# Kernel optimization log

Hardware: AMD Instinct MI355X
Metric: run time of the kernel (lower is better)

The kernel has to match this reference:

```python
import jax, jax.numpy as jnp
import numpy as np

TOP_K = 8
N_GROUP = 8
TOPK_GROUP = 4
ROUTED_SCALE = 2.5


def setup_inputs() -> dict:
    key = jax.random.key(0)
    ks = jax.random.split(key, 7)
    T, H, E, I, SI = 4096, 1024, 32, 512, 2048
    W = 0.05  # weight scale to keep relu^2 activations sane
    return {
        "hidden_states": jax.random.normal(ks[0], (T, H), jnp.float32),
        "gate_w": jax.random.normal(ks[1], (E, H), jnp.float32) * W,
        "bias": jax.random.normal(ks[2], (E,), jnp.float32),
        "w_up": jax.random.normal(ks[3], (E, I, H), jnp.float32) * W,
        "w_down": jax.random.normal(ks[4], (E, H, I), jnp.float32) * W,
        "shared_up": jax.random.normal(ks[5], (SI, H), jnp.float32) * W,
        "shared_down": jax.random.normal(ks[6], (H, SI), jnp.float32) * W,
    }


def _grouped_topk_sigmoid(logits, bias):
    # vLLM grouped_topk with scoring_func='sigmoid' + e_score_correction_bias
    T, E = logits.shape
    scores = jax.nn.sigmoid(logits)                       # [T, E]
    sfc = scores + bias[None, :]                          # scores for choice
    g = sfc.reshape(T, N_GROUP, E // N_GROUP)
    group_scores = jnp.sum(jax.lax.top_k(g, 2)[0], -1)    # [T, G] sum of top-2
    grp_idx = jax.lax.top_k(group_scores, TOPK_GROUP)[1]  # [T, topk_group]
    gmask = jnp.zeros((T, N_GROUP), bool).at[jnp.arange(T)[:, None], grp_idx].set(True)
    emask = jnp.repeat(gmask, E // N_GROUP, axis=1)       # [T, E]
    masked = jnp.where(emask, sfc, -jnp.inf)
    topk_ids = jax.lax.top_k(masked, TOP_K)[1]            # [T, K]
    topk_w = jnp.take_along_axis(scores, topk_ids, axis=1)  # weights from raw scores
    topk_w = topk_w / jnp.sum(topk_w, axis=-1, keepdims=True)  # renormalize
    return topk_w, topk_ids


def reference(hidden_states, gate_w, bias, w_up, w_down, shared_up, shared_down):
    x = hidden_states
    T, H = x.shape
    E = gate_w.shape[0]
    # router (fp32 gate)
    logits = x.astype(jnp.float32) @ gate_w.T
    topk_w, topk_ids = _grouped_topk_sigmoid(logits, bias)
    # dense combine weights [T, E] (zero for unselected experts)
    gates = jnp.zeros((T, E), x.dtype).at[jnp.arange(T)[:, None], topk_ids].set(
        topk_w.astype(x.dtype))
    # routed experts: relu^2 MLP (no gating mul), combined with gate weights
    h = jnp.einsum('th,eih->tei', x, w_up)                # [T, E, I]
    h = jnp.square(jax.nn.relu(h))
    routed = jnp.einsum('tei,te,ehi->th', h, gates, w_down)
    # shared expert (same relu^2 MLP)
    s = jnp.square(jax.nn.relu(x @ shared_up.T)) @ shared_down.T
    return routed * ROUTED_SCALE + s
```

## Files before the change

kernel.cpp:

```cpp
#include <hip/hip_runtime.h>
#include <hip/hip_bf16.h>


typedef _Float16 h8 __attribute__((ext_vector_type(8)));
typedef _Float16 h4 __attribute__((ext_vector_type(4)));
typedef float f4 __attribute__((ext_vector_type(4)));

#define T_TOK 4096
#define HDIM  1024
#define NEXP  32
#define IDIM  512
#define SIDIM 2048
#define TOPK  8
#define MAXTU 224
#define MAXTD 160

__device__ __forceinline__ void gload16(const void* g, void* l) {
    __builtin_amdgcn_global_load_lds(
        (const __attribute__((address_space(1))) void*)g,
        (__attribute__((address_space(3))) void*)l, 16, 0, 0);
}

__global__ __launch_bounds__(256) void cvt_all_kernel(
    const float* __restrict__ sA, _Float16* __restrict__ dA, int nA,
    const float* __restrict__ sB, _Float16* __restrict__ dB, int nB,
    const float* __restrict__ sC, _Float16* __restrict__ dC, int nC,
    const float* __restrict__ sD, _Float16* __restrict__ dD, int nD,
    const float* __restrict__ sE, _Float16* __restrict__ dE, int nE) {
    const int total = nA + nB + nC + nD + nE;
    for (int gi = blockIdx.x * 256 + threadIdx.x; gi < total; gi += gridDim.x * 256) {
        const float* s; _Float16* d; int i = gi;
        if (i < nA) { s = sA; d = dA; }
        else { i -= nA;
        if (i < nB) { s = sB; d = dB; }
        else { i -= nB;
        if (i < nC) { s = sC; d = dC; }
        else { i -= nC;
        if (i < nD) { s = sD; d = dD; }
        else { i -= nD; s = sE; d = dE; } } } }
        float4 v = reinterpret_cast<const float4*>(s)[i];
        h4 h; h[0] = (_Float16)v.x; h[1] = (_Float16)v.y; h[2] = (_Float16)v.z; h[3] = (_Float16)v.w;
        reinterpret_cast<h4*>(d)[i] = h;
    }
}

__global__ __launch_bounds__(256) void logits_select_kernel(
    const float* __restrict__ x, const float* __restrict__ gw,
    const float* __restrict__ bias, int* __restrict__ topk_ids,
    float* __restrict__ topk_w) {
    const int t0  = blockIdx.x * 16;
    const int tid = threadIdx.x;
    __shared__ double xS[16][66];
    __shared__ double gS[32][65];
    __shared__ double sS[16][33];
    __shared__ double sfcS[16][33];
    const int e  = tid & 31;
    const int tg = tid >> 5;
    const int tA = tg * 2, tB = tg * 2 + 1;
    double acc0 = 0.0, acc1 = 0.0;

    for (int kc = 0; kc < HDIM; kc += 64) {
        {
            int r = tid >> 4, c0 = (tid & 15) * 4;
            float4 v = *reinterpret_cast<const float4*>(x + (size_t)(t0 + r) * HDIM + kc + c0);
            xS[r][c0]     = (double)v.x;
            xS[r][c0 + 1] = (double)v.y;
            xS[r][c0 + 2] = (double)v.z;
            xS[r][c0 + 3] = (double)v.w;
        }
        {
            int r = tid >> 3, c0 = (tid & 7) * 8;
            const float* gp = gw + (size_t)r * HDIM + kc + c0;
            float4 v0 = *reinterpret_cast<const float4*>(gp);
            float4 v1 = *reinterpret_cast<const float4*>(gp + 4);
            gS[r][c0]     = (double)v0.x;
            gS[r][c0 + 1] = (double)v0.y;
            gS[r][c0 + 2] = (double)v0.z;
            gS[r][c0 + 3] = (double)v0.w;
            gS[r][c0 + 4] = (double)v1.x;
            gS[r][c0 + 5] = (double)v1.y;
            gS[r][c0 + 6] = (double)v1.z;
            gS[r][c0 + 7] = (double)v1.w;
        }
        __syncthreads();
#pragma unroll
        for (int k = 0; k < 64; ++k) {
            double g = gS[e][k];
            acc0 = fma(g, xS[tA][k], acc0);
            acc1 = fma(g, xS[tB][k], acc1);
        }
        __syncthreads();
    }
    {
        double s0 = 1.0 / (1.0 + exp(-acc0));
        double s1 = 1.0 / (1.0 + exp(-acc1));
        double b = (double)bias[e];
        sS[tA][e] = s0;  sfcS[tA][e] = s0 + b;
        sS[tB][e] = s1;  sfcS[tB][e] = s1 + b;
    }
    __syncthreads();

    if (tid < 16) {
        const int t = t0 + tid;
        double gsc[8];
        for (int g = 0; g < 8; ++g) {
            double m1 = -1e300, m2 = -1e300;
            for (int j = 0; j < 4; ++j) {
                double v = sfcS[tid][g * 4 + j];
                if (v > m1) { m2 = m1; m1 = v; } else if (v > m2) { m2 = v; }
            }
            gsc[g] = m1 + m2;
        }
        bool gsel[8] = {};
        for (int r = 0; r < 4; ++r) {
            int best = 0; double bv = -1e300;
            for (int g = 0; g < 8; ++g)
                if (!gsel[g] && gsc[g] > bv) { bv = gsc[g]; best = g; }
            gsel[best] = true;
        }
        bool esel[32];
        for (int i2 = 0; i2 < 32; ++i2) esel[i2] = false;
        int ids[8]; double wsum = 0.0;
        for (int r = 0; r < 8; ++r) {
            int best = 0; double bv = -1e300;
            for (int e2 = 0; e2 < 32; ++e2)
                if (gsel[e2 >> 2] && !esel[e2] && sfcS[tid][e2] > bv) { bv = sfcS[tid][e2]; best = e2; }
            esel[best] = true;
            ids[r] = best;
            wsum += sS[tid][best];
        }
        for (int r = 0; r < 8; ++r) {
            topk_ids[t * TOPK + r] = ids[r];
            topk_w[t * TOPK + r] = (float)(sS[tid][ids[r]] / wsum * 2.5);
        }
    }
}

__global__ void build_lists_kernel(const int* __restrict__ ids, const float* __restrict__ w,
                                   int* __restrict__ tok_list, float* __restrict__ wt_list,
                                   int* __restrict__ dest_list, int* __restrict__ counts) {
    const int e = blockIdx.x;
    const int lane = threadIdx.x;
    int base = 0;
    for (int t0 = 0; t0 < T_TOK; t0 += 64) {
        int t = t0 + lane;
        int found = -1;
#pragma unroll
        for (int k = 0; k < TOPK; ++k)
            if (ids[t * TOPK + k] == e) found = k;
        unsigned long long mask = __ballot(found >= 0);
        if (found >= 0) {
            int pos = base + __popcll(mask & ((1ull << lane) - 1ull));
            tok_list[e * T_TOK + pos]  = t;
            wt_list[e * T_TOK + pos]   = w[t * TOPK + found];
            dest_list[e * T_TOK + pos] = t * TOPK + found;
        }
        base += __popcll(mask);
    }
    if (lane == 0) counts[e] = base;
}

__global__ void scan_offsets_kernel(const int* __restrict__ counts, int* __restrict__ offsets,
                                    int* __restrict__ tmapU, int* __restrict__ tmapD) {
    if (threadIdx.x == 0) {
        int run = 0, ntu = 0, ntd = 0;
        for (int e = 0; e < NEXP; ++e) {
            offsets[e] = run;
            for (int m0 = 0; m0 < counts[e]; m0 += 256) {
                tmapU[1 + 2 * ntu] = e; tmapU[2 + 2 * ntu] = m0; ++ntu;
                tmapD[1 + 2 * ntd] = e; tmapD[2 + 2 * ntd] = m0; ++ntd;
            }
            run += counts[e];
        }
        offsets[NEXP] = run;
        for (int c = 0; c < 4; ++c)
            for (int m0 = 0; m0 < T_TOK; m0 += 256) {
                tmapU[1 + 2 * ntu] = NEXP + c; tmapU[2 + 2 * ntu] = m0; ++ntu;
            }
        tmapU[0] = ntu;
        tmapD[0] = ntd;
    }
}

__device__ __forceinline__ void gemm8p(const _Float16* const (&aP)[4],
                                       const _Float16* const (&bP)[4],
                                       const int nt, f4 (&acc)[8][4]) {
    __shared__ __attribute__((aligned(16))) _Float16 As[2][256 * 64];
    __shared__ __attribute__((aligned(16))) _Float16 Bs[2][256 * 64];
    const int tid = threadIdx.x;
    const int w = tid >> 6, lane = tid & 63;
    const int wr = w >> 2, wc = w & 3;
    const int ra = lane & 15, kq = lane >> 4;
    const int ldsb = w * 512;
    const int arow = wr * 128 + ra;
    const int brow = wc * 64 + ra;
    const int ch0 = (kq ^ (ra & 7)) << 3;
    const int ch1 = ((4 + kq) ^ (ra & 7)) << 3;

#pragma unroll
    for (int j = 0; j < 4; ++j) gload16(aP[j], &As[0][j * 4096 + ldsb]);
#pragma unroll
    for (int j = 0; j < 4; ++j) gload16(bP[j], &Bs[0][j * 4096 + ldsb]);

    for (int t = 0; t < nt; ++t) {
        const int buf = t & 1, nb = buf ^ 1;
        const bool pf = (t + 1 < nt);
        const int ko = (t + 1) * 64;

        asm volatile("s_waitcnt vmcnt(0)" ::: "memory");
        __builtin_amdgcn_s_barrier();
        asm volatile("" ::: "memory");

        h8 bf0[4], af0[4];
#pragma unroll
        for (int n = 0; n < 4; ++n)
            bf0[n] = *reinterpret_cast<const h8*>(&Bs[buf][(brow + n * 16) * 64 + ch0]);
#pragma unroll
        for (int m = 0; m < 4; ++m)
            af0[m] = *reinterpret_cast<const h8*>(&As[buf][(arow + m * 16) * 64 + ch0]);
        if (pf) {
            gload16(aP[0] + ko, &As[nb][0 * 4096 + ldsb]);
            gload16(aP[1] + ko, &As[nb][1 * 4096 + ldsb]);
        }
        h8 af1[4];
#pragma unroll
        for (int m = 0; m < 4; ++m)
            af1[m] = *reinterpret_cast<const h8*>(&As[buf][(arow + (m + 4) * 16) * 64 + ch0]);
        if (pf) {
            gload16(aP[2] + ko, &As[nb][2 * 4096 + ldsb]);
            gload16(aP[3] + ko, &As[nb][3 * 4096 + ldsb]);
        }
        __builtin_amdgcn_s_setprio(1);
#pragma unroll
        for (int m = 0; m < 4; ++m)
#pragma unroll
            for (int n = 0; n < 4; ++n)
                acc[m][n] = __builtin_amdgcn_mfma_f32_16x16x32_f16(af0[m], bf0[n], acc[m][n], 0, 0, 0);
        __builtin_amdgcn_s_setprio(0);
        if (pf) {
            gload16(bP[0] + ko, &Bs[nb][0 * 4096 + ldsb]);
            gload16(bP[1] + ko, &Bs[nb][1 * 4096 + ldsb]);
        }
        h8 bf1[4], af2[4];
#pragma unroll
        for (int n = 0; n < 4; ++n)
            bf1[n] = *reinterpret_cast<const h8*>(&Bs[buf][(brow + n * 16) * 64 + ch1]);
#pragma unroll
        for (int m = 0; m < 4; ++m)
            af2[m] = *reinterpret_cast<const h8*>(&As[buf][(arow + m * 16) * 64 + ch1]);
        __builtin_amdgcn_s_setprio(1);
#pragma unroll
        for (int m = 0; m < 4; ++m)
#pragma unroll
            for (int n = 0; n < 4; ++n)
                acc[m + 4][n] = __builtin_amdgcn_mfma_f32_16x16x32_f16(af1[m], bf0[n], acc[m + 4][n], 0, 0, 0);
        __builtin_amdgcn_s_setprio(0);
        if (pf) {
            gload16(bP[2] + ko, &Bs[nb][2 * 4096 + ldsb]);
            gload16(bP[3] + ko, &Bs[nb][3 * 4096 + ldsb]);
        }
        h8 af3[4];
#pragma unroll
        for (int m = 0; m < 4; ++m)
            af3[m] = *reinterpret_cast<const h8*>(&As[buf][(arow + (m + 4) * 16) * 64 + ch1]);
        __builtin_amdgcn_s_setprio(1);
#pragma unroll
        for (int m = 0; m < 4; ++m)
#pragma unroll
            for (int n = 0; n < 4; ++n)
                acc[m][n] = __builtin_amdgcn_mfma_f32_16x16x32_f16(af2[m], bf1[n], acc[m][n], 0, 0, 0);
#pragma unroll
        for (int m = 0; m < 4; ++m)
#pragma unroll
            for (int n = 0; n < 4; ++n)
                acc[m + 4][n] = __builtin_amdgcn_mfma_f32_16x16x32_f16(af3[m], bf1[n], acc[m + 4][n], 0, 0, 0);
        __builtin_amdgcn_s_setprio(0);

        asm volatile("" ::: "memory");
        __builtin_amdgcn_s_barrier();
        asm volatile("" ::: "memory");
    }
}

__global__ __launch_bounds__(512, 2) void up_kernel(
    const _Float16* __restrict__ xh, const _Float16* __restrict__ whup,
    const _Float16* __restrict__ shupW,
    const int* __restrict__ tok_list, const float* __restrict__ wt_list,
    const int* __restrict__ counts, const int* __restrict__ offsets,
    const int* __restrict__ tmap,
    _Float16* __restrict__ hbuf, _Float16* __restrict__ shb) {
    const int ti = blockIdx.x;
    if (ti >= tmap[0]) return;
    const int e  = tmap[1 + 2 * ti];
    const int m0 = tmap[2 + 2 * ti];
    const int n0 = blockIdx.y * 256;
    const bool routed = e < NEXP;
    const int cnt = routed ? counts[e] : T_TOK;

    __shared__ int   tokS[256];
    __shared__ float wS[256];
    const int tid = threadIdx.x;
    if (tid < 256) {
        int row = m0 + tid;
        int cr = row < cnt ? row : cnt - 1;
        if (routed) {
            tokS[tid] = tok_list[e * T_TOK + cr];
            wS[tid]   = row < cnt ? wt_list[e * T_TOK + row] : 0.f;
        } else {
            tokS[tid] = cr;
            wS[tid]   = 1.f;
        }
    }
    __syncthreads();

    const int w = tid >> 6, lane = tid & 63;
    const int swz = ((lane & 7) ^ (lane >> 3)) << 3;
    const int rr = w * 8 + (lane >> 3);
    const _Float16* bbase = routed ? (whup + (size_t)e * IDIM * HDIM)
                                   : (shupW + (size_t)(e - NEXP) * 512 * HDIM);
    const _Float16* aP[4]; const _Float16* bP[4];
#pragma unroll
    for (int j = 0; j < 4; ++j) {
        aP[j] = xh + (size_t)tokS[j * 64 + rr] * HDIM + swz;
        bP[j] = bbase + (size_t)(n0 + j * 64 + rr) * HDIM + swz;
    }
    f4 acc[8][4] = {};
    gemm8p(aP, bP, HDIM / 64, acc);

    const int wr = w >> 2, wc = w & 3;
    const int kq = lane >> 4, ra = lane & 15;
    _Float16* obase; size_t ostr;
    if (routed) { obase = hbuf + (size_t)(offsets[e] + m0) * IDIM + n0; ostr = IDIM; }
    else        { obase = shb + (size_t)m0 * SIDIM + (size_t)(e - NEXP) * 512 + n0; ostr = SIDIM; }
#pragma unroll
    for (int m = 0; m < 8; ++m)
#pragma unroll
    for (int r = 0; r < 4; ++r) {
        int orow = wr * 128 + m * 16 + kq * 4 + r;
        if (m0 + orow < cnt) {
            float g = wS[orow];
#pragma unroll
            for (int n = 0; n < 4; ++n) {
                float v = fmaxf(acc[m][n][r], 0.f);
                obase[(size_t)orow * ostr + wc * 64 + n * 16 + ra] = (_Float16)(v * v * g);
            }
        }
    }
}

template<bool SLOT>
__global__ __launch_bounds__(512, 2) void down_routed_kernel(
    const _Float16* __restrict__ hbuf, const _Float16* __restrict__ whdown,
    const int* __restrict__ dest_list, const int* __restrict__ counts,
    const int* __restrict__ offsets, const int* __restrict__ tmap,
    _Float16* __restrict__ slotout, float* __restrict__ out) {
    const int ti = blockIdx.x;
    if (ti >= tmap[0]) return;
    const int e   = tmap[1 + 2 * ti];
    const int m0  = tmap[2 + 2 * ti];
    const int cnt = counts[e];
    const int n0   = blockIdx.y * 256;
    const int eoff = offsets[e];

    __shared__ int dS[256];
    const int tid = threadIdx.x;
    if (tid < 256) {
        int row = m0 + tid;
        dS[tid] = dest_list[e * T_TOK + (row < cnt ? row : cnt - 1)];
    }
    __syncthreads();

    const int w = tid >> 6, lane = tid & 63;
    const int swz = ((lane & 7) ^ (lane >> 3)) << 3;
    const int rr = w * 8 + (lane >> 3);
    const _Float16* aP[4]; const _Float16* bP[4];
#pragma unroll
    for (int j = 0; j < 4; ++j) {
        int row = m0 + j * 64 + rr;
        int cr  = row < cnt ? row : cnt - 1;
        aP[j] = hbuf + (size_t)(eoff + cr) * IDIM + swz;
        bP[j] = whdown + ((size_t)e * HDIM + n0 + j * 64 + rr) * IDIM + swz;
    }
    f4 acc[8][4] = {};
    gemm8p(aP, bP, IDIM / 64, acc);

    const int wr = w >> 2, wc = w & 3;
    const int kq = lane >> 4, ra = lane & 15;
#pragma unroll
    for (int m = 0; m < 8; ++m)
#pragma unroll
    for (int r = 0; r < 4; ++r) {
        int orow = wr * 128 + m * 16 + kq * 4 + r;
        if (m0 + orow < cnt) {
            int d = dS[orow];
            if (SLOT) {
                size_t rb = (size_t)d * HDIM + n0;
#pragma unroll
                for (int n = 0; n < 4; ++n)
                    slotout[rb + wc * 64 + n * 16 + ra] = (_Float16)acc[m][n][r];
            } else {
                size_t rb = (size_t)(d >> 3) * HDIM + n0;
#pragma unroll
                for (int n = 0; n < 4; ++n)
                    atomicAdd(&out[rb + wc * 64 + n * 16 + ra], acc[m][n][r]);
            }
        }
    }
}

template<int K>
__device__ __forceinline__ void gemm128(const _Float16* const (&aSrc)[4],
                                        const _Float16* const (&bSrc)[4],
                                        f4 (&acc)[4][4]) {
    __shared__ __attribute__((aligned(16))) _Float16 As[128 * 64];
    __shared__ __attribute__((aligned(16))) _Float16 Bs[128 * 64];
    const int tid  = threadIdx.x;
    const int w    = tid >> 6, lane = tid & 63;
    const int wm   = (w & 1) * 64, wn = (w >> 1) * 64;
    const int ra   = lane & 15, kq = lane >> 4;

    for (int kk = 0; kk < K; kk += 64) {
#pragma unroll
        for (int i = 0; i < 4; ++i) {
            gload16(aSrc[i] + kk, As + (size_t)(i * 256 + w * 64) * 8);
            gload16(bSrc[i] + kk, Bs + (size_t)(i * 256 + w * 64) * 8);
        }
        __syncthreads();
#pragma unroll
        for (int s = 0; s < 2; ++s) {
            h8 af[4], bf[4];
#pragma unroll
            for (int m = 0; m < 4; ++m) {
                int row = wm + m * 16 + ra;
                af[m] = *reinterpret_cast<const h8*>(As + row * 64 + (((s * 4 + kq) ^ (row & 7)) << 3));
            }
#pragma unroll
            for (int n = 0; n < 4; ++n) {
                int row = wn + n * 16 + ra;
                bf[n] = *reinterpret_cast<const h8*>(Bs + row * 64 + (((s * 4 + kq) ^ (row & 7)) << 3));
            }
#pragma unroll
            for (int m = 0; m < 4; ++m)
#pragma unroll
                for (int n = 0; n < 4; ++n)
                    acc[m][n] = __builtin_amdgcn_mfma_f32_16x16x32_f16(af[m], bf[n], acc[m][n], 0, 0, 0);
        }
        __syncthreads();
    }
}

template<bool COMB>
__global__ __launch_bounds__(256) void down_shared_kernel(
    const _Float16* __restrict__ sh, const _Float16* __restrict__ shdown,
    const _Float16* __restrict__ slotout, float* __restrict__ out) {
    const int m0 = blockIdx.y * 128;
    const int n0 = blockIdx.x * 128;
    const int tid = threadIdx.x;
    const int sc = ((tid & 7) ^ ((tid >> 3) & 7)) << 3;
    const int r0 = tid >> 3;
    const _Float16* aSrc[4]; const _Float16* bSrc[4];
#pragma unroll
    for (int i = 0; i < 4; ++i) {
        aSrc[i] = sh + (size_t)(m0 + i * 32 + r0) * SIDIM + sc;
        bSrc[i] = shdown + (size_t)(n0 + i * 32 + r0) * SIDIM + sc;
    }
    f4 acc[4][4] = {};
    gemm128<SIDIM>(aSrc, bSrc, acc);

    const int w = tid >> 6, lane = tid & 63;
    const int wm = (w & 1) * 64, wn = (w >> 1) * 64;
    const int cq = lane >> 4, cc = lane & 15;
#pragma unroll
    for (int m = 0; m < 4; ++m)
#pragma unroll
    for (int r = 0; r < 4; ++r) {
        int orow = wm + m * 16 + cq * 4 + r;
        size_t trow = (size_t)(m0 + orow);
#pragma unroll
        for (int n = 0; n < 4; ++n) {
            int col = n0 + wn + n * 16 + cc;
            float v = acc[m][n][r];
            if (COMB) {
                const _Float16* sp = slotout + trow * TOPK * HDIM + col;
#pragma unroll
                for (int k = 0; k < TOPK; ++k)
                    v += (float)sp[(size_t)k * HDIM];
            }
            out[trow * HDIM + col] = v;
        }
    }
}

extern "C" void kernel_launch(void* const* d_in, const int* in_sizes, int n_in,
                              void* d_out, int out_size, void* d_ws, size_t ws_size,
                              hipStream_t stream) {
    const float* x     = (const float*)d_in[0];
    const float* gw    = (const float*)d_in[1];
    const float* bias  = (const float*)d_in[2];
    const float* wup   = (const float*)d_in[3];
    const float* wdown = (const float*)d_in[4];
    const float* sup   = (const float*)d_in[5];
    const float* sdown = (const float*)d_in[6];
    float* out = (float*)d_out;

    char* ws = (char*)d_ws;
    size_t off = 0;
    auto take = [&](size_t bytes) {
        char* p = ws + off;
        off = (off + bytes + 255) & ~(size_t)255;
        return p;
    };
    _Float16* xh      = (_Float16*)take((size_t)T_TOK * HDIM * 2);
    _Float16* whup    = (_Float16*)take((size_t)NEXP * IDIM * HDIM * 2);
    _Float16* whdown  = (_Float16*)take((size_t)NEXP * HDIM * IDIM * 2);
    _Float16* shupW   = (_Float16*)take((size_t)SIDIM * HDIM * 2);
    _Float16* shdownW = (_Float16*)take((size_t)HDIM * SIDIM * 2);
    _Float16* sh      = (_Float16*)take((size_t)T_TOK * SIDIM * 2);
    _Float16* hbuf    = (_Float16*)take((size_t)T_TOK * TOPK * IDIM * 2);
    int*   ids       = (int*)take((size_t)T_TOK * TOPK * 4);
    float* tw        = (float*)take((size_t)T_TOK * TOPK * 4);
    int*   tok_list  = (int*)take((size_t)NEXP * T_TOK * 4);
    float* wt_list   = (float*)take((size_t)NEXP * T_TOK * 4);
    int*   dest_list = (int*)take((size_t)NEXP * T_TOK * 4);
    int*   counts    = (int*)take(NEXP * 4);
    int*   offsets   = (int*)take((NEXP + 1) * 4);
    int*   tmapU     = (int*)take((1 + 2 * MAXTU) * 4);
    int*   tmapD     = (int*)take((1 + 2 * MAXTD) * 4);
    _Float16* slotout = (_Float16*)take((size_t)T_TOK * TOPK * HDIM * 2);
    const bool use_slot = off <= ws_size;

    logits_select_kernel<<<T_TOK / 16, 256, 0, stream>>>(x, gw, bias, ids, tw);
    build_lists_kernel<<<NEXP, 64, 0, stream>>>(ids, tw, tok_list, wt_list, dest_list, counts);
    scan_offsets_kernel<<<1, 64, 0, stream>>>(counts, offsets, tmapU, tmapD);

    cvt_all_kernel<<<2048, 256, 0, stream>>>(
        x, xh, T_TOK * HDIM / 4,
        wup, whup, NEXP * IDIM * HDIM / 4,
        wdown, whdown, NEXP * HDIM * IDIM / 4,
        sup, shupW, SIDIM * HDIM / 4,
        sdown, shdownW, HDIM * SIDIM / 4);

    up_kernel<<<dim3(MAXTU, 2), 512, 0, stream>>>(
        xh, whup, shupW, tok_list, wt_list, counts, offsets, tmapU, hbuf, sh);

    if (use_slot) {
        down_routed_kernel<true><<<dim3(MAXTD, HDIM / 256), 512, 0, stream>>>(
            hbuf, whdown, dest_list, counts, offsets, tmapD, slotout, out);
        down_shared_kernel<true><<<dim3(HDIM / 128, T_TOK / 128), 256, 0, stream>>>(
            sh, shdownW, slotout, out);
    } else {
        down_shared_kernel<false><<<dim3(HDIM / 128, T_TOK / 128), 256, 0, stream>>>(
            sh, shdownW, slotout, out);
        down_routed_kernel<false><<<dim3(MAXTD, HDIM / 256), 512, 0, stream>>>(
            hbuf, whdown, dest_list, counts, offsets, tmapD, slotout, out);
    }
}
```

Before: 316.4 us.

## Prefetch two K-tiles ahead and split GEMM loop into barrier-synced phases

Reworks the double-buffered GEMM main loop so that tile t+2 is issued right after tile t is consumed, with a partial vmcnt(8) wait letting the next tile's loads stay in flight. Each iteration is split into four phases of LDS fragment loads followed by a barrier and MFMA block, which lockstep waves so LDS reads and MFMA bursts alternate across the block. This aims to hide global-load latency more deeply and cut LDS and MFMA contention, at the cost of more barriers per iteration, and relies on the vmcnt count matching exactly eight outstanding loads.

```diff
diff --git a/kernel.cpp b/kernel.cpp
--- a/kernel.cpp
+++ b/kernel.cpp
@@ -197,17 +197,31 @@
     const int ch0 = (kq ^ (ra & 7)) << 3;
     const int ch1 = ((4 + kq) ^ (ra & 7)) << 3;
 
-#pragma unroll
-    for (int j = 0; j < 4; ++j) gload16(aP[j], &As[0][j * 4096 + ldsb]);
-#pragma unroll
-    for (int j = 0; j < 4; ++j) gload16(bP[j], &Bs[0][j * 4096 + ldsb]);
+#define STAGE8(tt, bb) do {                                         \
+        const int _ko = (tt) * 64;                                  \
+        _Pragma("unroll")                                           \
+        for (int _j = 0; _j < 4; ++_j) {                            \
+            gload16(aP[_j] + _ko, &As[bb][_j * 4096 + ldsb]);       \
+            gload16(bP[_j] + _ko, &Bs[bb][_j * 4096 + ldsb]);       \
+        } } while (0)
+
+#define PHASE_SYNC()                                                \
+        asm volatile("" ::: "memory");                              \
+        __builtin_amdgcn_s_barrier();                               \
+        asm volatile("s_waitcnt lgkmcnt(0)" ::: "memory")
+
+#define PHASE_END()                                                 \
+        asm volatile("" ::: "memory");                              \
+        __builtin_amdgcn_s_barrier();                               \
+        asm volatile("" ::: "memory")
+
+    STAGE8(0, 0);
+    if (nt > 1) STAGE8(1, 1);
 
     for (int t = 0; t < nt; ++t) {
-        const int buf = t & 1, nb = buf ^ 1;
-        const bool pf = (t + 1 < nt);
-        const int ko = (t + 1) * 64;
-
-        asm volatile("s_waitcnt vmcnt(0)" ::: "memory");
+        const int buf = t & 1;
+        if (t + 1 < nt) asm volatile("s_waitcnt vmcnt(8)" ::: "memory");
+        else            asm volatile("s_waitcnt vmcnt(0)" ::: "memory");
         __builtin_amdgcn_s_barrier();
         asm volatile("" ::: "memory");
 
@@ -218,18 +232,7 @@
 #pragma unroll
         for (int m = 0; m < 4; ++m)
             af0[m] = *reinterpret_cast<const h8*>(&As[buf][(arow + m * 16) * 64 + ch0]);
-        if (pf) {
-            gload16(aP[0] + ko, &As[nb][0 * 4096 + ldsb]);
-            gload16(aP[1] + ko, &As[nb][1 * 4096 + ldsb]);
-        }
-        h8 af1[4];
-#pragma unroll
-        for (int m = 0; m < 4; ++m)
-            af1[m] = *reinterpret_cast<const h8*>(&As[buf][(arow + (m + 4) * 16) * 64 + ch0]);
-        if (pf) {
-            gload16(aP[2] + ko, &As[nb][2 * 4096 + ldsb]);
-            gload16(aP[3] + ko, &As[nb][3 * 4096 + ldsb]);
-        }
+        PHASE_SYNC();
         __builtin_amdgcn_s_setprio(1);
 #pragma unroll
         for (int m = 0; m < 4; ++m)
@@ -237,17 +240,13 @@
             for (int n = 0; n < 4; ++n)
                 acc[m][n] = __builtin_amdgcn_mfma_f32_16x16x32_f16(af0[m], bf0[n], acc[m][n], 0, 0, 0);
         __builtin_amdgcn_s_setprio(0);
-        if (pf) {
-            gload16(bP[0] + ko, &Bs[nb][0 * 4096 + ldsb]);
-            gload16(bP[1] + ko, &Bs[nb][1 * 4096 + ldsb]);
-        }
-        h8 bf1[4], af2[4];
-#pragma unroll
-        for (int n = 0; n < 4; ++n)
-            bf1[n] = *reinterpret_cast<const h8*>(&Bs[buf][(brow + n * 16) * 64 + ch1]);
-#pragma unroll
-        for (int m = 0; m < 4; ++m)
-            af2[m] = *reinterpret_cast<const h8*>(&As[buf][(arow + m * 16) * 64 + ch1]);
+        PHASE_END();
+
+        h8 af1[4];
+#pragma unroll
+        for (int m = 0; m < 4; ++m)
+            af1[m] = *reinterpret_cast<const h8*>(&As[buf][(arow + (m + 4) * 16) * 64 + ch0]);
+        PHASE_SYNC();
         __builtin_amdgcn_s_setprio(1);
 #pragma unroll
         for (int m = 0; m < 4; ++m)
@@ -255,31 +254,44 @@
             for (int n = 0; n < 4; ++n)
                 acc[m + 4][n] = __builtin_amdgcn_mfma_f32_16x16x32_f16(af1[m], bf0[n], acc[m + 4][n], 0, 0, 0);
         __builtin_amdgcn_s_setprio(0);
-        if (pf) {
-            gload16(bP[2] + ko, &Bs[nb][2 * 4096 + ldsb]);
-            gload16(bP[3] + ko, &Bs[nb][3 * 4096 + ldsb]);
-        }
-        h8 af3[4];
-#pragma unroll
-        for (int m = 0; m < 4; ++m)
-            af3[m] = *reinterpret_cast<const h8*>(&As[buf][(arow + (m + 4) * 16) * 64 + ch1]);
+        PHASE_END();
+
+        h8 bf1[4], af2[4];
+#pragma unroll
+        for (int n = 0; n < 4; ++n)
+            bf1[n] = *reinterpret_cast<const h8*>(&Bs[buf][(brow + n * 16) * 64 + ch1]);
+#pragma unroll
+        for (int m = 0; m < 4; ++m)
+            af2[m] = *reinterpret_cast<const h8*>(&As[buf][(arow + m * 16) * 64 + ch1]);
+        PHASE_SYNC();
         __builtin_amdgcn_s_setprio(1);
 #pragma unroll
         for (int m = 0; m < 4; ++m)
 #pragma unroll
             for (int n = 0; n < 4; ++n)
                 acc[m][n] = __builtin_amdgcn_mfma_f32_16x16x32_f16(af2[m], bf1[n], acc[m][n], 0, 0, 0);
+        __builtin_amdgcn_s_setprio(0);
+        PHASE_END();
+
+        h8 af3[4];
+#pragma unroll
+        for (int m = 0; m < 4; ++m)
+            af3[m] = *reinterpret_cast<const h8*>(&As[buf][(arow + (m + 4) * 16) * 64 + ch1]);
+        PHASE_SYNC();
+        __builtin_amdgcn_s_setprio(1);
 #pragma unroll
         for (int m = 0; m < 4; ++m)
 #pragma unroll
             for (int n = 0; n < 4; ++n)
                 acc[m + 4][n] = __builtin_amdgcn_mfma_f32_16x16x32_f16(af3[m], bf1[n], acc[m + 4][n], 0, 0, 0);
         __builtin_amdgcn_s_setprio(0);
-
-        asm volatile("" ::: "memory");
-        __builtin_amdgcn_s_barrier();
-        asm volatile("" ::: "memory");
-    }
+        PHASE_END();
+
+        if (t + 2 < nt) STAGE8(t + 2, buf);
+    }
+#undef STAGE8
+#undef PHASE_SYNC
+#undef PHASE_END
 }
 
 __global__ __launch_bounds__(512, 2) void up_kernel(
```

After: 334.0 us. 1.06x slower.

## Fuse fp32-to-fp16 weight conversion into up/down GEMM B-operand staging

Applied to the files above, without the earlier changes.

Drops the separate conversion pass for routed up/down and shared-up weights. The GEMM tiles now load those weights as fp32 from global memory into registers, convert them to fp16 in-kernel and write them to swizzled LDS, replacing the direct global-to-LDS loads. This removes a large extra read and write of weight memory, but each tile re-reads fp32 weights at twice the bytes. It also adds register pressure and conversion ALU work inside the MFMA loop, plus extra lgkmcnt waits.

```diff
diff --git a/kernel.cpp b/kernel.cpp
--- a/kernel.cpp
+++ b/kernel.cpp
@@ -21,23 +21,20 @@
         (__attribute__((address_space(3))) void*)l, 16, 0, 0);
 }
 
-__global__ __launch_bounds__(256) void cvt_all_kernel(
+__device__ __forceinline__ h8 cvt8(const float4 a, const float4 b) {
+    h8 r;
+    r[0] = (_Float16)a.x; r[1] = (_Float16)a.y; r[2] = (_Float16)a.z; r[3] = (_Float16)a.w;
+    r[4] = (_Float16)b.x; r[5] = (_Float16)b.y; r[6] = (_Float16)b.z; r[7] = (_Float16)b.w;
+    return r;
+}
+
+__global__ __launch_bounds__(256) void cvt2_kernel(
     const float* __restrict__ sA, _Float16* __restrict__ dA, int nA,
-    const float* __restrict__ sB, _Float16* __restrict__ dB, int nB,
-    const float* __restrict__ sC, _Float16* __restrict__ dC, int nC,
-    const float* __restrict__ sD, _Float16* __restrict__ dD, int nD,
-    const float* __restrict__ sE, _Float16* __restrict__ dE, int nE) {
-    const int total = nA + nB + nC + nD + nE;
+    const float* __restrict__ sB, _Float16* __restrict__ dB, int nB) {
+    const int total = nA + nB;
     for (int gi = blockIdx.x * 256 + threadIdx.x; gi < total; gi += gridDim.x * 256) {
         const float* s; _Float16* d; int i = gi;
-        if (i < nA) { s = sA; d = dA; }
-        else { i -= nA;
-        if (i < nB) { s = sB; d = dB; }
-        else { i -= nB;
-        if (i < nC) { s = sC; d = dC; }
-        else { i -= nC;
-        if (i < nD) { s = sD; d = dD; }
-        else { i -= nD; s = sE; d = dE; } } } }
+        if (i < nA) { s = sA; d = dA; } else { i -= nA; s = sB; d = dB; }
         float4 v = reinterpret_cast<const float4*>(s)[i];
         h4 h; h[0] = (_Float16)v.x; h[1] = (_Float16)v.y; h[2] = (_Float16)v.z; h[3] = (_Float16)v.w;
         reinterpret_cast<h4*>(d)[i] = h;
@@ -183,7 +180,7 @@
 }
 
 __device__ __forceinline__ void gemm8p(const _Float16* const (&aP)[4],
-                                       const _Float16* const (&bP)[4],
+                                       const float* __restrict__ bp,
                                        const int nt, f4 (&acc)[8][4]) {
     __shared__ __attribute__((aligned(16))) _Float16 As[2][256 * 64];
     __shared__ __attribute__((aligned(16))) _Float16 Bs[2][256 * 64];
@@ -196,11 +193,27 @@
     const int brow = wc * 64 + ra;
     const int ch0 = (kq ^ (ra & 7)) << 3;
     const int ch1 = ((4 + kq) ^ (ra & 7)) << 3;
-
+    const int srow = tid >> 1;
+    const int shalf = tid & 1;
+
+#define BSTAGE_WRITE(bb) do {                                              \
+        _Pragma("unroll")                                                  \
+        for (int _c = 0; _c < 4; ++_c) {                                   \
+            h8 _hb = cvt8(bl[2 * _c], bl[2 * _c + 1]);                     \
+            int _gc = (shalf * 4 + _c) ^ (srow & 7);                       \
+            *reinterpret_cast<h8*>(&Bs[bb][srow * 64 + _gc * 8]) = _hb;    \
+        } } while (0)
+
+    {
+        float4 bl[8];
+#pragma unroll
+        for (int c = 0; c < 8; ++c)
+            bl[c] = *reinterpret_cast<const float4*>(bp + c * 4);
+        BSTAGE_WRITE(0);
+    }
 #pragma unroll
     for (int j = 0; j < 4; ++j) gload16(aP[j], &As[0][j * 4096 + ldsb]);
-#pragma unroll
-    for (int j = 0; j < 4; ++j) gload16(bP[j], &Bs[0][j * 4096 + ldsb]);
+    asm volatile("s_waitcnt lgkmcnt(0)" ::: "memory");
 
     for (int t = 0; t < nt; ++t) {
         const int buf = t & 1, nb = buf ^ 1;
@@ -211,6 +224,13 @@
         __builtin_amdgcn_s_barrier();
         asm volatile("" ::: "memory");
 
+        float4 bl[8];
+        if (pf) {
+#pragma unroll
+            for (int c = 0; c < 8; ++c)
+                bl[c] = *reinterpret_cast<const float4*>(bp + ko + c * 4);
+        }
+
         h8 bf0[4], af0[4];
 #pragma unroll
         for (int n = 0; n < 4; ++n)
@@ -237,10 +257,6 @@
             for (int n = 0; n < 4; ++n)
                 acc[m][n] = __builtin_amdgcn_mfma_f32_16x16x32_f16(af0[m], bf0[n], acc[m][n], 0, 0, 0);
         __builtin_amdgcn_s_setprio(0);
-        if (pf) {
-            gload16(bP[0] + ko, &Bs[nb][0 * 4096 + ldsb]);
-            gload16(bP[1] + ko, &Bs[nb][1 * 4096 + ldsb]);
-        }
         h8 bf1[4], af2[4];
 #pragma unroll
         for (int n = 0; n < 4; ++n)
@@ -255,10 +271,7 @@
             for (int n = 0; n < 4; ++n)
                 acc[m + 4][n] = __builtin_amdgcn_mfma_f32_16x16x32_f16(af1[m], bf0[n], acc[m + 4][n], 0, 0, 0);
         __builtin_amdgcn_s_setprio(0);
-        if (pf) {
-            gload16(bP[2] + ko, &Bs[nb][2 * 4096 + ldsb]);
-            gload16(bP[3] + ko, &Bs[nb][3 * 4096 + ldsb]);
-        }
+        if (pf) BSTAGE_WRITE(nb);
         h8 af3[4];
 #pragma unroll
         for (int m = 0; m < 4; ++m)
@@ -276,15 +289,16 @@
                 acc[m + 4][n] = __builtin_amdgcn_mfma_f32_16x16x32_f16(af3[m], bf1[n], acc[m + 4][n], 0, 0, 0);
         __builtin_amdgcn_s_setprio(0);
 
-        asm volatile("" ::: "memory");
+        asm volatile("s_waitcnt lgkmcnt(0)" ::: "memory");
         __builtin_amdgcn_s_barrier();
         asm volatile("" ::: "memory");
     }
+#undef BSTAGE_WRITE
 }
 
 __global__ __launch_bounds__(512, 2) void up_kernel(
-    const _Float16* __restrict__ xh, const _Float16* __restrict__ whup,
-    const _Float16* __restrict__ shupW,
+    const _Float16* __restrict__ xh, const float* __restrict__ wup,
+    const float* __restrict__ sup,
     const int* __restrict__ tok_list, const float* __restrict__ wt_list,
     const int* __restrict__ counts, const int* __restrict__ offsets,
     const int* __restrict__ tmap,
@@ -316,16 +330,16 @@
     const int w = tid >> 6, lane = tid & 63;
     const int swz = ((lane & 7) ^ (lane >> 3)) << 3;
     const int rr = w * 8 + (lane >> 3);
-    const _Float16* bbase = routed ? (whup + (size_t)e * IDIM * HDIM)
-                                   : (shupW + (size_t)(e - NEXP) * 512 * HDIM);
-    const _Float16* aP[4]; const _Float16* bP[4];
-#pragma unroll
-    for (int j = 0; j < 4; ++j) {
+    const float* bbase = routed ? (wup + (size_t)e * IDIM * HDIM)
+                                : (sup + (size_t)(e - NEXP) * 512 * HDIM);
+    const float* bp = bbase + (size_t)(n0 + (tid >> 1)) * HDIM + (tid & 1) * 32;
+    const _Float16* aP[4];
+#pragma unroll
+    for (int j = 0; j < 4; ++j)
         aP[j] = xh + (size_t)tokS[j * 64 + rr] * HDIM + swz;
-        bP[j] = bbase + (size_t)(n0 + j * 64 + rr) * HDIM + swz;
-    }
+
     f4 acc[8][4] = {};
-    gemm8p(aP, bP, HDIM / 64, acc);
+    gemm8p(aP, bp, HDIM / 64, acc);
 
     const int wr = w >> 2, wc = w & 3;
     const int kq = lane >> 4, ra = lane & 15;
@@ -350,7 +364,7 @@
 
 template<bool SLOT>
 __global__ __launch_bounds__(512, 2) void down_routed_kernel(
-    const _Float16* __restrict__ hbuf, const _Float16* __restrict__ whdown,
+    const _Float16* __restrict__ hbuf, const float* __restrict__ wdown,
     const int* __restrict__ dest_list, const int* __restrict__ counts,
     const int* __restrict__ offsets, const int* __restrict__ tmap,
     _Float16* __restrict__ slotout, float* __restrict__ out) {
@@ -373,16 +387,16 @@
     const int w = tid >> 6, lane = tid & 63;
     const int swz = ((lane & 7) ^ (lane >> 3)) << 3;
     const int rr = w * 8 + (lane >> 3);
-    const _Float16* aP[4]; const _Float16* bP[4];
+    const float* bp = wdown + ((size_t)e * HDIM + n0 + (tid >> 1)) * IDIM + (tid & 1) * 32;
+    const _Float16* aP[4];
 #pragma unroll
     for (int j = 0; j < 4; ++j) {
         int row = m0 + j * 64 + rr;
         int cr  = row < cnt ? row : cnt - 1;
         aP[j] = hbuf + (size_t)(eoff + cr) * IDIM + swz;
-        bP[j] = whdown + ((size_t)e * HDIM + n0 + j * 64 + rr) * IDIM + swz;
     }
     f4 acc[8][4] = {};
-    gemm8p(aP, bP, IDIM / 64, acc);
+    gemm8p(aP, bp, IDIM / 64, acc);
 
     const int wr = w >> 2, wc = w & 3;
     const int kq = lane >> 4, ra = lane & 15;
@@ -511,9 +525,6 @@
         return p;
     };
     _Float16* xh      = (_Float16*)take((size_t)T_TOK * HDIM * 2);
-    _Float16* whup    = (_Float16*)take((size_t)NEXP * IDIM * HDIM * 2);
-    _Float16* whdown  = (_Float16*)take((size_t)NEXP * HDIM * IDIM * 2);
-    _Float16* shupW   = (_Float16*)take((size_t)SIDIM * HDIM * 2);
     _Float16* shdownW = (_Float16*)take((size_t)HDIM * SIDIM * 2);
     _Float16* sh      = (_Float16*)take((size_t)T_TOK * SIDIM * 2);
     _Float16* hbuf    = (_Float16*)take((size_t)T_TOK * TOPK * IDIM * 2);
@@ -533,25 +544,22 @@
     build_lists_kernel<<<NEXP, 64, 0, stream>>>(ids, tw, tok_list, wt_list, dest_list, counts);
     scan_offsets_kernel<<<1, 64, 0, stream>>>(counts, offsets, tmapU, tmapD);
 
-    cvt_all_kernel<<<2048, 256, 0, stream>>>(
+    cvt2_kernel<<<2048, 256, 0, stream>>>(
         x, xh, T_TOK * HDIM / 4,
-        wup, whup, NEXP * IDIM * HDIM / 4,
-        wdown, whdown, NEXP * HDIM * IDIM / 4,
-        sup, shupW, SIDIM * HDIM / 4,
         sdown, shdownW, HDIM * SIDIM / 4);
 
     up_kernel<<<dim3(MAXTU, 2), 512, 0, stream>>>(
-        xh, whup, shupW, tok_list, wt_list, counts, offsets, tmapU, hbuf, sh);
+        xh, wup, sup, tok_list, wt_list, counts, offsets, tmapU, hbuf, sh);
 
     if (use_slot) {
         down_routed_kernel<true><<<dim3(MAXTD, HDIM / 256), 512, 0, stream>>>(
-            hbuf, whdown, dest_list, counts, offsets, tmapD, slotout, out);
+            hbuf, wdown, dest_list, counts, offsets, tmapD, slotout, out);
         down_shared_kernel<true><<<dim3(HDIM / 128, T_TOK / 128), 256, 0, stream>>>(
             sh, shdownW, slotout, out);
     } else {
         down_shared_kernel<false><<<dim3(HDIM / 128, T_TOK / 128), 256, 0, stream>>>(
             sh, shdownW, slotout, out);
         down_routed_kernel<false><<<dim3(MAXTD, HDIM / 256), 512, 0, stream>>>(
-            hbuf, whdown, dest_list, counts, offsets, tmapD, slotout, out);
-    }
-}
+            hbuf, wdown, dest_list, counts, offsets, tmapD, slotout, out);
+    }
+}
```

After: 410.9 us. 1.3x slower.
